# Kernel optimization log

Measured on AMD Instinct MI355X. Metric: run time of the kernel, lower is better.

## Reference

```python
import jax, jax.numpy as jnp
import numpy as np

B, S, H = 16, 4096, 1152
GRID = 64  # 64x64 patch grid -> S = GRID*GRID
OUT_LEN = 256  # pooled soft tokens (k = sqrt(S/OUT_LEN) = 4)


def setup_inputs() -> dict:
    key = jax.random.key(0)
    x = jax.random.normal(key, (B, S, H), dtype=jnp.float32)
    i = jnp.arange(S)
    # position_ids[..., 0] = x coord, [..., 1] = y coord on the patch grid
    pos = jnp.stack([i % GRID, i // GRID], axis=-1).astype(jnp.int32)  # [S, 2]
    position_ids = jnp.broadcast_to(pos, (B, S, 2))
    return {"x": x, "position_ids": position_ids, "output_length": OUT_LEN}


def reference(x, position_ids, output_length):
    b, s, h = x.shape
    # zero out padding positions (pos == [-1, -1])
    padding = jnp.all(position_ids == -1, axis=-1)  # [B, S]
    x = jnp.where(padding[..., None], jnp.float32(0.0), x)

    k = int((s // output_length) ** 0.5)
    k2 = k * k

    pos = jnp.maximum(position_ids, 0)
    max_x = jnp.max(pos[..., 0], axis=-1, keepdims=True) + 1  # [B, 1]
    # bucket index of each patch: (x//k) + (max_x//k) * (y//k)
    kidx = pos[..., 0] // k + (max_x // k) * pos[..., 1] // 1 * 0 + (pos[..., 0] // k) * 0 + (pos[..., 0] // k)
    kidx = pos[..., 0] // k + (max_x // k) * (pos[..., 1] // k)  # [B, S]

    # scatter-mean: segment_sum over flattened (batch-offset) bucket ids, / k^2
    seg = (kidx + jnp.arange(b)[:, None] * output_length).reshape(-1)
    pooled = jax.ops.segment_sum(
        x.reshape(b * s, h), seg, num_segments=b * output_length
    ).reshape(b, output_length, h) / jnp.float32(k2)

    root_hidden = jnp.float32(h ** 0.5)
    return pooled * root_hidden
```

## Files before the change

kernel.cpp:

```cpp
#include <hip/hip_runtime.h>


#define BB 16
#define SS 4096
#define HH 1152
#define OUTL 256
#define KK 4
#define K2 16
#define H4 (HH / 4)
#define HP (H4 / 2)

__global__ __launch_bounds__(256) void build_fused(const int* __restrict__ pos,
                                                   int* __restrict__ counts,
                                                   int* __restrict__ rows) {
    int b = blockIdx.x;
    int t = threadIdx.x;
    const int2* p2 = reinterpret_cast<const int2*>(pos) + (size_t)b * SS;

    int m = 0;
    for (int s = t; s < SS; s += 256) m = max(m, p2[s].x);
    __shared__ int red[256];
    red[t] = m;
    __syncthreads();
    for (int w = 128; w > 0; w >>= 1) {
        if (t < w) red[t] = max(red[t], red[t + w]);
        __syncthreads();
    }
    __shared__ int smxk;
    if (t == 0) smxk = (red[0] + 1) / KK;

    __shared__ int lrows[OUTL * K2];
#pragma unroll
    for (int i = 0; i < K2; ++i) lrows[t + i * 256] = -1;
    __syncthreads();
    int mxk = smxk;
    for (int s = t; s < SS; s += 256) {
        int2 xy = p2[s];
        if (xy.x == -1 && xy.y == -1) continue;
        int px = max(xy.x, 0), py = max(xy.y, 0);
        int kidx = px / KK + mxk * (py / KK);
        int slot = (py & (KK - 1)) * KK + (px & (KK - 1));
        if ((unsigned)kidx < OUTL) lrows[kidx * K2 + slot] = s;
    }
    __syncthreads();

    int* rb = rows + ((size_t)b * OUTL + t) * K2;
    int c = 0;
#pragma unroll
    for (int j = 0; j < K2; ++j) {
        int v = lrows[t * K2 + j];
        if (v >= 0) rb[c++] = v;
    }
    counts[b * OUTL + t] = c;
}

__global__ __launch_bounds__(256) void gather_kernel(const float* __restrict__ x,
                                                     const int* __restrict__ counts,
                                                     const int* __restrict__ rows,
                                                     float* __restrict__ out) {
    int idx = blockIdx.x * 256 + threadIdx.x;
    int c = idx % HP;
    int bo = idx / HP;
    int b = bo >> 8;

    const float4* xb = reinterpret_cast<const float4*>(x) + (size_t)b * SS * H4 + c;
    const int* rl = rows + (size_t)bo * K2;
    int cnt = min(counts[bo], K2);

    float4 a0 = {0.f, 0.f, 0.f, 0.f};
    float4 a1 = {0.f, 0.f, 0.f, 0.f};
    if (cnt == K2) {
        const int4* rl4 = reinterpret_cast<const int4*>(rl);
        int4 ra = rl4[0], rb_ = rl4[1], rc = rl4[2], rd = rl4[3];
        int ridx[K2] = {ra.x, ra.y, ra.z, ra.w, rb_.x, rb_.y, rb_.z, rb_.w,
                        rc.x, rc.y, rc.z, rc.w, rd.x, rd.y, rd.z, rd.w};
#pragma unroll
        for (int j = 0; j < K2; ++j) {
            const float4* p = xb + (size_t)ridx[j] * H4;
            float4 v0 = p[0], v1 = p[HP];
            a0.x += v0.x; a0.y += v0.y; a0.z += v0.z; a0.w += v0.w;
            a1.x += v1.x; a1.y += v1.y; a1.z += v1.z; a1.w += v1.w;
        }
    } else {
        for (int j = 0; j < cnt; ++j) {
            const float4* p = xb + (size_t)rl[j] * H4;
            float4 v0 = p[0], v1 = p[HP];
            a0.x += v0.x; a0.y += v0.y; a0.z += v0.z; a0.w += v0.w;
            a1.x += v1.x; a1.y += v1.y; a1.z += v1.z; a1.w += v1.w;
        }
    }
    const float scale = 2.1213203435596424f;
    a0.x *= scale; a0.y *= scale; a0.z *= scale; a0.w *= scale;
    a1.x *= scale; a1.y *= scale; a1.z *= scale; a1.w *= scale;
    float4* ob = reinterpret_cast<float4*>(out) + (size_t)bo * H4 + c;
    ob[0] = a0;
    ob[HP] = a1;
}

extern "C" void kernel_launch(void* const* d_in, const int* in_sizes, int n_in,
                              void* d_out, int out_size, void* d_ws, size_t ws_size,
                              hipStream_t stream) {
    const float* x = (const float*)d_in[0];
    const int* pos = (const int*)d_in[1];
    float* out = (float*)d_out;

    int* counts = (int*)d_ws;
    int* rows = counts + BB * OUTL;

    build_fused<<<BB, 256, 0, stream>>>(pos, counts, rows);

    int total = BB * OUTL * HP;
    gather_kernel<<<total / 256, 256, 0, stream>>>(x, counts, rows, out);
}
```

Before: 66.34 us.

## Fuse bucket-index build into gather kernel, recomputing row lists per block

Merges the two launches into one kernel. Each block reloads the batch's position ids (32 KB), computes the max x with a wavefront-shuffle reduction, and builds row lists only for the up-to-three output buckets it covers. The gather then reads indices from shared memory. This removes a kernel launch, the serialization between the two kernels, and the workspace round trip. In exchange, every one of the 2304 blocks redundantly rereads position_ids and recomputes bucket indices, which adds L2 traffic and work before each block can start its x loads.

After: 60.94 us. -8.1%, faster.

```diff
diff --git a/kernel.cpp b/kernel.cpp
--- a/kernel.cpp
+++ b/kernel.cpp
@@ -9,81 +9,64 @@
 #define K2 16
 #define H4 (HH / 4)
 #define HP (H4 / 2)
+#define BPB 144
+#define NB 3
 
-__global__ __launch_bounds__(256) void build_fused(const int* __restrict__ pos,
-                                                   int* __restrict__ counts,
-                                                   int* __restrict__ rows) {
-    int b = blockIdx.x;
+__global__ __launch_bounds__(256) void pool_fused(const float* __restrict__ x,
+                                                  const int* __restrict__ pos,
+                                                  float* __restrict__ out) {
+    int blk = blockIdx.x;
+    int b = blk / BPB;
+    int bl = blk - b * BPB;
     int t = threadIdx.x;
+    int lidx = bl * 256 + t;
+    int bo_local = lidx / HP;
+    int c = lidx - bo_local * HP;
+    int lo = (bl * 256) / HP;
+
     const int2* p2 = reinterpret_cast<const int2*>(pos) + (size_t)b * SS;
 
+    int2 rr[SS / 256];
+#pragma unroll
+    for (int i = 0; i < SS / 256; ++i) rr[i] = p2[t + i * 256];
+
     int m = 0;
-    for (int s = t; s < SS; s += 256) m = max(m, p2[s].x);
-    __shared__ int red[256];
-    red[t] = m;
+#pragma unroll
+    for (int i = 0; i < SS / 256; ++i) m = max(m, rr[i].x);
+#pragma unroll
+    for (int o = 32; o > 0; o >>= 1) m = max(m, __shfl_down(m, o));
+
+    __shared__ int wred[4];
+    __shared__ int lrows[NB * K2];
+    if ((t & 63) == 0) wred[t >> 6] = m;
+    if (t < NB * K2) lrows[t] = -1;
     __syncthreads();
-    for (int w = 128; w > 0; w >>= 1) {
-        if (t < w) red[t] = max(red[t], red[t + w]);
-        __syncthreads();
-    }
-    __shared__ int smxk;
-    if (t == 0) smxk = (red[0] + 1) / KK;
+    int mxk = (max(max(wred[0], wred[1]), max(wred[2], wred[3])) + 1) / KK;
 
-    __shared__ int lrows[OUTL * K2];
 #pragma unroll
-    for (int i = 0; i < K2; ++i) lrows[t + i * 256] = -1;
-    __syncthreads();
-    int mxk = smxk;
-    for (int s = t; s < SS; s += 256) {
-        int2 xy = p2[s];
+    for (int i = 0; i < SS / 256; ++i) {
+        int2 xy = rr[i];
         if (xy.x == -1 && xy.y == -1) continue;
         int px = max(xy.x, 0), py = max(xy.y, 0);
         int kidx = px / KK + mxk * (py / KK);
-        int slot = (py & (KK - 1)) * KK + (px & (KK - 1));
-        if ((unsigned)kidx < OUTL) lrows[kidx * K2 + slot] = s;
+        unsigned rel = (unsigned)(kidx - lo);
+        if (rel < NB) lrows[rel * K2 + (py & (KK - 1)) * KK + (px & (KK - 1))] = t + i * 256;
     }
     __syncthreads();
 
-    int* rb = rows + ((size_t)b * OUTL + t) * K2;
-    int c = 0;
+    int rel = bo_local - lo;
+    int ridx[K2];
+#pragma unroll
+    for (int j = 0; j < K2; ++j) ridx[j] = lrows[rel * K2 + j];
+
+    const float4* xb = reinterpret_cast<const float4*>(x) + (size_t)b * SS * H4 + c;
+    float4 a0 = {0.f, 0.f, 0.f, 0.f};
+    float4 a1 = {0.f, 0.f, 0.f, 0.f};
 #pragma unroll
     for (int j = 0; j < K2; ++j) {
-        int v = lrows[t * K2 + j];
-        if (v >= 0) rb[c++] = v;
-    }
-    counts[b * OUTL + t] = c;
-}
-
-__global__ __launch_bounds__(256) void gather_kernel(const float* __restrict__ x,
-                                                     const int* __restrict__ counts,
-                                                     const int* __restrict__ rows,
-                                                     float* __restrict__ out) {
-    int idx = blockIdx.x * 256 + threadIdx.x;
-    int c = idx % HP;
-    int bo = idx / HP;
-    int b = bo >> 8;
-
-    const float4* xb = reinterpret_cast<const float4*>(x) + (size_t)b * SS * H4 + c;
-    const int* rl = rows + (size_t)bo * K2;
-    int cnt = min(counts[bo], K2);
-
-    float4 a0 = {0.f, 0.f, 0.f, 0.f};
-    float4 a1 = {0.f, 0.f, 0.f, 0.f};
-    if (cnt == K2) {
-        const int4* rl4 = reinterpret_cast<const int4*>(rl);
-        int4 ra = rl4[0], rb_ = rl4[1], rc = rl4[2], rd = rl4[3];
-        int ridx[K2] = {ra.x, ra.y, ra.z, ra.w, rb_.x, rb_.y, rb_.z, rb_.w,
-                        rc.x, rc.y, rc.z, rc.w, rd.x, rd.y, rd.z, rd.w};
-#pragma unroll
-        for (int j = 0; j < K2; ++j) {
-            const float4* p = xb + (size_t)ridx[j] * H4;
-            float4 v0 = p[0], v1 = p[HP];
-            a0.x += v0.x; a0.y += v0.y; a0.z += v0.z; a0.w += v0.w;
-            a1.x += v1.x; a1.y += v1.y; a1.z += v1.z; a1.w += v1.w;
-        }
-    } else {
-        for (int j = 0; j < cnt; ++j) {
-            const float4* p = xb + (size_t)rl[j] * H4;
+        int row = ridx[j];
+        if (row >= 0) {
+            const float4* p = xb + (size_t)row * H4;
             float4 v0 = p[0], v1 = p[HP];
             a0.x += v0.x; a0.y += v0.y; a0.z += v0.z; a0.w += v0.w;
             a1.x += v1.x; a1.y += v1.y; a1.z += v1.z; a1.w += v1.w;
@@ -92,6 +75,8 @@
     const float scale = 2.1213203435596424f;
     a0.x *= scale; a0.y *= scale; a0.z *= scale; a0.w *= scale;
     a1.x *= scale; a1.y *= scale; a1.z *= scale; a1.w *= scale;
+
+    int bo = b * OUTL + bo_local;
     float4* ob = reinterpret_cast<float4*>(out) + (size_t)bo * H4 + c;
     ob[0] = a0;
     ob[HP] = a1;
@@ -104,11 +89,5 @@
     const int* pos = (const int*)d_in[1];
     float* out = (float*)d_out;
 
-    int* counts = (int*)d_ws;
-    int* rows = counts + BB * OUTL;
-
-    build_fused<<<BB, 256, 0, stream>>>(pos, counts, rows);
-
-    int total = BB * OUTL * HP;
-    gather_kernel<<<total / 256, 256, 0, stream>>>(x, counts, rows, out);
+    pool_fused<<<BB * BPB, 256, 0, stream>>>(x, pos, out);
 }
```
